# Kernel optimization log

Hardware: AMD Instinct MI355X
Metric: run time of the kernel (lower is better)

The kernel has to match this reference:

```python
import jax, jax.numpy as jnp
import numpy as np

B, T, D, H = 2, 2048, 1024, 16
HD = D // H  # head_dim = 64


def setup_inputs() -> dict:
    key = jax.random.key(0)
    ks = jax.random.split(key, 9)
    s = 0.02
    return {
        "hidden_states": jax.random.normal(ks[0], (B, T, D), jnp.float32),
        "attention_mask": jnp.zeros((B, 1, T, T), jnp.float32),
        "Wq": jax.random.normal(ks[1], (D, D), jnp.float32) * s,
        "bq": jax.random.normal(ks[2], (D,), jnp.float32) * s,
        "Wk": jax.random.normal(ks[3], (D, D), jnp.float32) * s,
        "bk": jax.random.normal(ks[4], (D,), jnp.float32) * s,
        "Wv": jax.random.normal(ks[5], (D, D), jnp.float32) * s,
        "bv": jax.random.normal(ks[6], (D,), jnp.float32) * s,
        "Wo": jax.random.normal(ks[7], (D, D), jnp.float32) * s,
        "bo": jax.random.normal(ks[8], (D,), jnp.float32) * s,
    }


def _heads(x):
    # [B, T, D] -> [B, H, T, HD]
    return x.reshape(B, -1, H, HD).transpose(0, 2, 1, 3)


def reference(hidden_states, attention_mask, Wq, bq, Wk, bk, Wv, bv, Wo, bo):
    scaling = HD ** -0.5
    # nn.Linear: x @ W.T + b; query scaled BEFORE head split (as in source)
    q = _heads((hidden_states @ Wq.T + bq) * scaling)  # [B,H,T,HD]
    k = _heads(hidden_states @ Wk.T + bk)
    v = _heads(hidden_states @ Wv.T + bv)
    # eager QK^T -> +mask -> softmax -> @V (full [B,H,T,T] materialized)
    attn = jnp.einsum('bhqd,bhkd->bhqk', q, k) + attention_mask
    attn = jax.nn.softmax(attn, axis=-1)
    out = jnp.einsum('bhqk,bhkd->bhqd', attn, v)  # [B,H,T,HD]
    out = out.transpose(0, 2, 1, 3).reshape(B, -1, D)
    return out @ Wo.T + bo
```

## Files before the change

kernel.cpp:

```cpp
#include <hip/hip_runtime.h>
#include <hip/hip_bf16.h>

typedef __bf16 v8bf __attribute__((ext_vector_type(8)));
typedef unsigned short v8us __attribute__((ext_vector_type(8)));
typedef float v4f __attribute__((ext_vector_type(4)));

#define B_ 2
#define T_ 2048
#define D_ 1024
#define H_ 16
#define HD_ 64
#define M_ 4096
#define LDST 88
#define PSTR 72

static __device__ __forceinline__ unsigned short f2bfbits(float f) {
    __hip_bfloat16 h = __float2bfloat16(f);
    unsigned short u;
    __builtin_memcpy(&u, &h, 2);
    return u;
}

static __device__ __forceinline__ v8us load8_f32_to_bf16(const float* g) {
    float4 fa = *(const float4*)g;
    float4 fb = *(const float4*)(g + 4);
    v8us p;
    p[0] = f2bfbits(fa.x); p[1] = f2bfbits(fa.y);
    p[2] = f2bfbits(fa.z); p[3] = f2bfbits(fa.w);
    p[4] = f2bfbits(fb.x); p[5] = f2bfbits(fb.y);
    p[6] = f2bfbits(fb.z); p[7] = f2bfbits(fb.w);
    return p;
}

static __device__ __forceinline__ void async16(const void* g, void* l) {
    __builtin_amdgcn_global_load_lds(
        (const __attribute__((address_space(1))) void*)g,
        (__attribute__((address_space(3))) void*)l, 16, 0, 0);
}

__global__ __launch_bounds__(256) void cvt_f32_bf16(
    const float* __restrict__ src, __hip_bfloat16* __restrict__ dst) {
    int i = (blockIdx.x * 256 + threadIdx.x) * 8;
    *(v8us*)&dst[i] = load8_f32_to_bf16(&src[i]);
}

__global__ __launch_bounds__(256) void gemm_qkv(
    const __hip_bfloat16* __restrict__ A, const __hip_bfloat16* __restrict__ W,
    const float* __restrict__ bq_, const float* __restrict__ bk_,
    const float* __restrict__ bv_, __hip_bfloat16* __restrict__ qo,
    __hip_bfloat16* __restrict__ ko, __hip_bfloat16* __restrict__ vo) {
    __shared__ __hip_bfloat16 sA[128 * 64];
    __shared__ __hip_bfloat16 sW[128 * 64];
    const int tid = threadIdx.x;
    const int wid = tid >> 6, lane = tid & 63;
    const int quad = lane >> 4, lq = lane & 15;
    const int wm = wid & 1, wn = wid >> 1;
    const int n0 = blockIdx.x * 128, m0 = blockIdx.y * 128;
    const int mid = n0 >> 10;
    const float* bias = (mid == 0) ? bq_ : (mid == 1) ? bk_ : bv_;

    v4f acc[4][4] = {};

    for (int k0 = 0; k0 < 1024; k0 += 64) {
        __syncthreads();
        for (int it = 0; it < 8; ++it) {
            int Lc = it * 256 + tid;
            int l1 = Lc & 1023;
            int row = l1 >> 3, pos = l1 & 7;
            if (it < 4)
                async16(&A[(size_t)(m0 + row) * 1024 + k0 + ((pos ^ (row & 7)) * 8)],
                        &sA[l1 * 8]);
            else
                async16(&W[(size_t)(n0 + row) * 1024 + k0 + ((pos ^ (row & 7)) * 8)],
                        &sW[l1 * 8]);
        }
        __syncthreads();
        for (int c = 0; c < 2; ++c) {
            v8bf af[4], wf[4];
            for (int mf = 0; mf < 4; ++mf) {
                int row = wm * 64 + mf * 16 + lq;
                af[mf] = *(const v8bf*)&sA[row * 64 + (((c * 4 + quad) ^ (lq & 7)) * 8)];
            }
            for (int nf = 0; nf < 4; ++nf) {
                int row = wn * 64 + nf * 16 + lq;
                wf[nf] = *(const v8bf*)&sW[row * 64 + (((c * 4 + quad) ^ (lq & 7)) * 8)];
            }
            for (int mf = 0; mf < 4; ++mf)
                for (int nf = 0; nf < 4; ++nf)
                    acc[mf][nf] = __builtin_amdgcn_mfma_f32_16x16x32_bf16(
                        af[mf], wf[nf], acc[mf][nf], 0, 0, 0);
        }
    }

    for (int nf = 0; nf < 4; ++nf) {
        int n = n0 + wn * 64 + nf * 16 + lq;
        int nl = n & 1023;
        int hh = nl >> 6, dd = nl & 63;
        float bvv = bias[nl];
        for (int mf = 0; mf < 4; ++mf) {
            int mbase = m0 + wm * 64 + mf * 16 + quad * 4;
            int bb = mbase >> 11;
            if (mid == 2) {
                int t0 = mbase & 2047;
                ushort4 pk;
                pk.x = f2bfbits(acc[mf][nf][0] + bvv);
                pk.y = f2bfbits(acc[mf][nf][1] + bvv);
                pk.z = f2bfbits(acc[mf][nf][2] + bvv);
                pk.w = f2bfbits(acc[mf][nf][3] + bvv);
                *(ushort4*)&vo[(((size_t)(bb * H_ + hh)) * HD_ + dd) * T_ + t0] = pk;
            } else {
                __hip_bfloat16* dst = (mid == 0) ? qo : ko;
                float sc = (mid == 0) ? 0.125f : 1.0f;
                for (int r = 0; r < 4; ++r) {
                    int m = mbase + r;
                    int t = m & 2047;
                    dst[(((size_t)(bb * H_ + hh)) * T_ + t) * HD_ + dd] =
                        __float2bfloat16((acc[mf][nf][r] + bvv) * sc);
                }
            }
        }
    }
}

__global__ __launch_bounds__(256) void gemm_out(
    const __hip_bfloat16* __restrict__ A, const __hip_bfloat16* __restrict__ W,
    const float* __restrict__ bias, float* __restrict__ out) {
    __shared__ __hip_bfloat16 sA[128 * 64];
    __shared__ __hip_bfloat16 sW[64 * 64];
    const int tid = threadIdx.x;
    const int wid = tid >> 6, lane = tid & 63;
    const int quad = lane >> 4, lq = lane & 15;
    const int wm = wid & 1, wn = wid >> 1;
    const int n0 = blockIdx.x * 64, m0 = blockIdx.y * 128;

    v4f acc[4][2] = {};

    for (int k0 = 0; k0 < 1024; k0 += 64) {
        __syncthreads();
        for (int it = 0; it < 4; ++it) {
            int Lc = wid * 256 + it * 64 + lane;
            int row = Lc >> 3, pos = Lc & 7;
            async16(&A[(size_t)(m0 + row) * 1024 + k0 + ((pos ^ (row & 7)) * 8)],
                    &sA[Lc * 8]);
        }
        for (int it = 0; it < 2; ++it) {
            int Lc = wid * 128 + it * 64 + lane;
            int row = Lc >> 3, pos = Lc & 7;
            async16(&W[(size_t)(n0 + row) * 1024 + k0 + ((pos ^ (row & 7)) * 8)],
                    &sW[Lc * 8]);
        }
        __syncthreads();
        for (int c = 0; c < 2; ++c) {
            v8bf af[4], wf[2];
            for (int mf = 0; mf < 4; ++mf) {
                int row = wm * 64 + mf * 16 + lq;
                af[mf] = *(const v8bf*)&sA[row * 64 + (((c * 4 + quad) ^ (lq & 7)) * 8)];
            }
            for (int nf = 0; nf < 2; ++nf) {
                int row = wn * 32 + nf * 16 + lq;
                wf[nf] = *(const v8bf*)&sW[row * 64 + (((c * 4 + quad) ^ (lq & 7)) * 8)];
            }
            for (int mf = 0; mf < 4; ++mf)
                for (int nf = 0; nf < 2; ++nf)
                    acc[mf][nf] = __builtin_amdgcn_mfma_f32_16x16x32_bf16(
                        af[mf], wf[nf], acc[mf][nf], 0, 0, 0);
        }
    }
    for (int nf = 0; nf < 2; ++nf) {
        int n = n0 + wn * 32 + nf * 16 + lq;
        float bv = bias[n];
        for (int mf = 0; mf < 4; ++mf) {
            int mbase = m0 + wm * 64 + mf * 16 + quad * 4;
            for (int r = 0; r < 4; ++r)
                out[(size_t)(mbase + r) * 1024 + n] = acc[mf][nf][r] + bv;
        }
    }
}

template <int EPI, bool ABF16, bool WBF16>
__global__ __launch_bounds__(256) void gemm128(
    const void* __restrict__ Av, const void* __restrict__ Wv_,
    const float* __restrict__ bias, void* __restrict__ outv) {
    __shared__ __hip_bfloat16 sA[128 * LDST];
    __shared__ __hip_bfloat16 sW[128 * LDST];
    const int tid = threadIdx.x;
    const int wid = tid >> 6, lane = tid & 63;
    const int quad = lane >> 4, lq = lane & 15;
    const int wm = wid & 1, wn = wid >> 1;
    const int n0 = blockIdx.x * 128, m0 = blockIdx.y * 128;
    v4f acc[4][4] = {};
    for (int k0 = 0; k0 < 1024; k0 += 64) {
        __syncthreads();
        for (int i = 0; i < 4; ++i) {
            int f = i * 256 + tid;
            int row = f >> 3, ch = f & 7;
            if constexpr (ABF16) {
                const __hip_bfloat16* A = (const __hip_bfloat16*)Av;
                *(int4*)&sA[row * LDST + ch * 8] =
                    *(const int4*)&A[(size_t)(m0 + row) * 1024 + k0 + ch * 8];
            } else {
                const float* A = (const float*)Av;
                *(v8us*)&sA[row * LDST + ch * 8] =
                    load8_f32_to_bf16(&A[(size_t)(m0 + row) * 1024 + k0 + ch * 8]);
            }
            if constexpr (WBF16) {
                const __hip_bfloat16* W = (const __hip_bfloat16*)Wv_;
                *(int4*)&sW[row * LDST + ch * 8] =
                    *(const int4*)&W[(size_t)(n0 + row) * 1024 + k0 + ch * 8];
            } else {
                const float* W = (const float*)Wv_;
                *(v8us*)&sW[row * LDST + ch * 8] =
                    load8_f32_to_bf16(&W[(size_t)(n0 + row) * 1024 + k0 + ch * 8]);
            }
        }
        __syncthreads();
        for (int c = 0; c < 2; ++c) {
            v8bf af[4], wf[4];
            for (int mf = 0; mf < 4; ++mf)
                af[mf] = *(const v8bf*)&sA[(wm * 64 + mf * 16 + lq) * LDST + c * 32 + quad * 8];
            for (int nf = 0; nf < 4; ++nf)
                wf[nf] = *(const v8bf*)&sW[(wn * 64 + nf * 16 + lq) * LDST + c * 32 + quad * 8];
            for (int mf = 0; mf < 4; ++mf)
                for (int nf = 0; nf < 4; ++nf)
                    acc[mf][nf] = __builtin_amdgcn_mfma_f32_16x16x32_bf16(
                        af[mf], wf[nf], acc[mf][nf], 0, 0, 0);
        }
    }
    for (int nf = 0; nf < 4; ++nf) {
        int n = n0 + wn * 64 + nf * 16 + lq;
        float bv = bias[n];
        for (int mf = 0; mf < 4; ++mf) {
            int mbase = m0 + wm * 64 + mf * 16 + quad * 4;
            if constexpr (EPI == 2) {
                __hip_bfloat16* out = (__hip_bfloat16*)outv;
                int bb = mbase >> 11, t0 = mbase & 2047;
                int hh = n >> 6, dd = n & 63;
                ushort4 pk;
                pk.x = f2bfbits(acc[mf][nf][0] + bv);
                pk.y = f2bfbits(acc[mf][nf][1] + bv);
                pk.z = f2bfbits(acc[mf][nf][2] + bv);
                pk.w = f2bfbits(acc[mf][nf][3] + bv);
                *(ushort4*)&out[(((size_t)(bb * H_ + hh)) * HD_ + dd) * T_ + t0] = pk;
            } else {
                for (int r = 0; r < 4; ++r) {
                    int m = mbase + r;
                    float v = acc[mf][nf][r] + bv;
                    if constexpr (EPI == 0) {
                        __hip_bfloat16* out = (__hip_bfloat16*)outv;
                        v *= 0.125f;
                        int bb = m >> 11, t = m & 2047, hh = n >> 6, dd = n & 63;
                        out[(((size_t)(bb * H_ + hh)) * T_ + t) * HD_ + dd] = __float2bfloat16(v);
                    } else if constexpr (EPI == 1) {
                        __hip_bfloat16* out = (__hip_bfloat16*)outv;
                        int bb = m >> 11, t = m & 2047, hh = n >> 6, dd = n & 63;
                        out[(((size_t)(bb * H_ + hh)) * T_ + t) * HD_ + dd] = __float2bfloat16(v);
                    } else {
                        float* out = (float*)outv;
                        out[(size_t)m * 1024 + n] = v;
                    }
                }
            }
        }
    }
}

__global__ __launch_bounds__(256) void attn_kernel(
    const __hip_bfloat16* __restrict__ q, const __hip_bfloat16* __restrict__ k,
    const __hip_bfloat16* __restrict__ vt, const float* __restrict__ mask,
    __hip_bfloat16* __restrict__ out) {
    __shared__ __hip_bfloat16 sK[64 * 64];
    __shared__ __hip_bfloat16 sV[64 * 64];
    __shared__ __hip_bfloat16 pT[4][32 * PSTR];
    const int tid = threadIdx.x;
    const int wid = tid >> 6, lane = tid & 63;
    const int quad = lane >> 4, lq = lane & 15;
    const int bh = blockIdx.y;
    const int b = bh >> 4, h = bh & 15;
    const int qb = blockIdx.x * 128 + wid * 32;
    const int qt0 = qb + lq, qt1 = qt0 + 16;

    v8bf bq0[2], bq1[2];
    for (int c = 0; c < 2; ++c) {
        bq0[c] = *(const v8bf*)&q[((size_t)bh * T_ + qt0) * HD_ + c * 32 + quad * 8];
        bq1[c] = *(const v8bf*)&q[((size_t)bh * T_ + qt1) * HD_ + c * 32 + quad * 8];
    }
    const float* mrow0 = mask + ((size_t)b * T_ + qt0) * T_;
    const float* mrow1 = mask + ((size_t)b * T_ + qt1) * T_;
    const __hip_bfloat16* kbase = k + (size_t)bh * T_ * HD_;
    const __hip_bfloat16* vbase = vt + (size_t)bh * HD_ * T_;

    float l0 = 0.f, l1 = 0.f;
    v4f o0[4] = {}, o1[4] = {};

    for (int kt0 = 0; kt0 < T_; kt0 += 64) {
        float4 mg0[4], mg1[4];
        for (int ki = 0; ki < 4; ++ki) {
            mg0[ki] = *(const float4*)&mrow0[kt0 + ki * 16 + quad * 4];
            mg1[ki] = *(const float4*)&mrow1[kt0 + ki * 16 + quad * 4];
        }
        __syncthreads();
        for (int it = 0; it < 2; ++it) {
            int Lc = wid * 128 + it * 64 + lane;
            int row = Lc >> 3, pos = Lc & 7;
            async16(&kbase[(size_t)(kt0 + row) * HD_ + ((pos ^ (row & 7)) * 8)],
                    &sK[Lc * 8]);
        }
        for (int it = 0; it < 2; ++it) {
            int Lc = wid * 128 + it * 64 + lane;
            int row = Lc >> 3, pos = Lc & 7;
            async16(&vbase[(size_t)row * T_ + kt0 + ((pos ^ (row & 7)) * 8)],
                    &sV[Lc * 8]);
        }
        __syncthreads();

        v4f st0[4] = {}, st1[4] = {};
        for (int ki = 0; ki < 4; ++ki)
            for (int c = 0; c < 2; ++c) {
                int row = ki * 16 + lq;
                v8bf ka = *(const v8bf*)&sK[row * 64 + (((c * 4 + quad) ^ (lq & 7)) * 8)];
                st0[ki] = __builtin_amdgcn_mfma_f32_16x16x32_bf16(ka, bq0[c], st0[ki], 0, 0, 0);
                st1[ki] = __builtin_amdgcn_mfma_f32_16x16x32_bf16(ka, bq1[c], st1[ki], 0, 0, 0);
            }
        for (int ki = 0; ki < 4; ++ki)
            for (int r = 0; r < 4; ++r) {
                st0[ki][r] = __expf(st0[ki][r] + (&mg0[ki].x)[r]);
                st1[ki][r] = __expf(st1[ki][r] + (&mg1[ki].x)[r]);
                l0 += st0[ki][r];
                l1 += st1[ki][r];
            }
        for (int ki = 0; ki < 4; ++ki) {
            ushort4 p0, p1;
            p0.x = f2bfbits(st0[ki][0]); p0.y = f2bfbits(st0[ki][1]);
            p0.z = f2bfbits(st0[ki][2]); p0.w = f2bfbits(st0[ki][3]);
            p1.x = f2bfbits(st1[ki][0]); p1.y = f2bfbits(st1[ki][1]);
            p1.z = f2bfbits(st1[ki][2]); p1.w = f2bfbits(st1[ki][3]);
            *(ushort4*)&pT[wid][lq * PSTR + ki * 16 + quad * 4] = p0;
            *(ushort4*)&pT[wid][(16 + lq) * PSTR + ki * 16 + quad * 4] = p1;
        }
        for (int c = 0; c < 2; ++c) {
            v8bf pb0 = *(const v8bf*)&pT[wid][lq * PSTR + c * 32 + quad * 8];
            v8bf pb1 = *(const v8bf*)&pT[wid][(16 + lq) * PSTR + c * 32 + quad * 8];
            for (int nt = 0; nt < 4; ++nt) {
                int row = nt * 16 + lq;
                v8bf va = *(const v8bf*)&sV[row * 64 + (((c * 4 + quad) ^ (lq & 7)) * 8)];
                o0[nt] = __builtin_amdgcn_mfma_f32_16x16x32_bf16(va, pb0, o0[nt], 0, 0, 0);
                o1[nt] = __builtin_amdgcn_mfma_f32_16x16x32_bf16(va, pb1, o1[nt], 0, 0, 0);
            }
        }
    }

    l0 += __shfl_xor(l0, 16); l0 += __shfl_xor(l0, 32);
    l1 += __shfl_xor(l1, 16); l1 += __shfl_xor(l1, 32);
    float i0 = 1.0f / l0, i1 = 1.0f / l1;
    for (int nt = 0; nt < 4; ++nt) {
        ushort4 p0, p1;
        p0.x = f2bfbits(o0[nt][0] * i0); p0.y = f2bfbits(o0[nt][1] * i0);
        p0.z = f2bfbits(o0[nt][2] * i0); p0.w = f2bfbits(o0[nt][3] * i0);
        p1.x = f2bfbits(o1[nt][0] * i1); p1.y = f2bfbits(o1[nt][1] * i1);
        p1.z = f2bfbits(o1[nt][2] * i1); p1.w = f2bfbits(o1[nt][3] * i1);
        *(ushort4*)&out[((size_t)b * T_ + qt0) * D_ + h * HD_ + nt * 16 + quad * 4] = p0;
        *(ushort4*)&out[((size_t)b * T_ + qt1) * D_ + h * HD_ + nt * 16 + quad * 4] = p1;
    }
}

extern "C" void kernel_launch(void* const* d_in, const int* in_sizes, int n_in,
                              void* d_out, int out_size, void* d_ws, size_t ws_size,
                              hipStream_t stream) {
    const float* hs   = (const float*)d_in[0];
    const float* mask = (const float*)d_in[1];
    const float* Wq   = (const float*)d_in[2];
    const float* bq   = (const float*)d_in[3];
    const float* Wk   = (const float*)d_in[4];
    const float* bk   = (const float*)d_in[5];
    const float* Wv   = (const float*)d_in[6];
    const float* bv   = (const float*)d_in[7];
    const float* Wo   = (const float*)d_in[8];
    const float* bo   = (const float*)d_in[9];
    float* out = (float*)d_out;

    const size_t TEN = (size_t)B_ * H_ * T_ * HD_;
    const size_t WEL = (size_t)D_ * D_;
    __hip_bfloat16* q_ws  = (__hip_bfloat16*)d_ws;
    __hip_bfloat16* k_ws  = q_ws + TEN;
    __hip_bfloat16* vt_ws = k_ws + TEN;
    __hip_bfloat16* at_ws = vt_ws + TEN;

    dim3 qkvgrid(3072 / 128, M_ / 128);
    dim3 outgrid(D_ / 64, M_ / 128);
    dim3 ogrid(D_ / 128, M_ / 128);
    dim3 agrid(T_ / 128, B_ * H_);

    const size_t need = (4 * TEN + TEN + 4 * WEL) * sizeof(__hip_bfloat16);
    if (ws_size >= need) {
        __hip_bfloat16* hsb = at_ws + TEN;
        __hip_bfloat16* wqb = hsb + TEN;
        __hip_bfloat16* wkb = wqb + WEL;
        __hip_bfloat16* wvb = wkb + WEL;
        __hip_bfloat16* wob = wvb + WEL;
        cvt_f32_bf16<<<(int)(TEN / 2048), 256, 0, stream>>>(hs, hsb);
        cvt_f32_bf16<<<(int)(WEL / 2048), 256, 0, stream>>>(Wq, wqb);
        cvt_f32_bf16<<<(int)(WEL / 2048), 256, 0, stream>>>(Wk, wkb);
        cvt_f32_bf16<<<(int)(WEL / 2048), 256, 0, stream>>>(Wv, wvb);
        cvt_f32_bf16<<<(int)(WEL / 2048), 256, 0, stream>>>(Wo, wob);
        gemm_qkv<<<qkvgrid, 256, 0, stream>>>(hsb, wqb, bq, bk, bv, q_ws, k_ws, vt_ws);
        attn_kernel<<<agrid, 256, 0, stream>>>(q_ws, k_ws, vt_ws, mask, at_ws);
        gemm_out<<<outgrid, 256, 0, stream>>>(at_ws, wob, bo, out);
    } else {
        gemm128<0, false, false><<<ogrid, 256, 0, stream>>>(hs, Wq, bq, q_ws);
        gemm128<1, false, false><<<ogrid, 256, 0, stream>>>(hs, Wk, bk, k_ws);
        gemm128<2, false, false><<<ogrid, 256, 0, stream>>>(hs, Wv, bv, vt_ws);
        attn_kernel<<<agrid, 256, 0, stream>>>(q_ws, k_ws, vt_ws, mask, at_ws);
        gemm128<3, true, false><<<ogrid, 256, 0, stream>>>(at_ws, Wo, bo, out);
    }
}
```

Baseline: 258.1 us.

## Enlarge attention KV tile to 128, fold log2e into Q, merge conversion launches

Each attention iteration now stages 128 keys and values in LDS instead of 64, which halves the number of barrier and load phases per query block. The inner loop is split into two 64-key halves, and the second half's mask is loaded after the first barrier to hide latency. The softmax scale now includes log2(e) in Q, so exp2f with an fma on the mask replaces __expf. The five f32-to-bf16 conversion launches are merged into one kernel. This costs twice the K/V LDS, which may lower occupancy, and the softmax still skips the running-max subtraction, so it could overflow on larger inputs.

Measured after the change: 262.5 us. No clear change (+1.7%).

```diff
diff --git a/kernel.cpp b/kernel.cpp
--- a/kernel.cpp
+++ b/kernel.cpp
@@ -13,6 +13,7 @@
 #define M_ 4096
 #define LDST 88
 #define PSTR 72
+#define LOG2E 1.44269504f
 
 static __device__ __forceinline__ unsigned short f2bfbits(float f) {
     __hip_bfloat16 h = __float2bfloat16(f);
@@ -38,9 +39,25 @@
         (__attribute__((address_space(3))) void*)l, 16, 0, 0);
 }
 
-__global__ __launch_bounds__(256) void cvt_f32_bf16(
-    const float* __restrict__ src, __hip_bfloat16* __restrict__ dst) {
-    int i = (blockIdx.x * 256 + threadIdx.x) * 8;
+__global__ __launch_bounds__(256) void cvt_multi(
+    const float* __restrict__ hs, const float* __restrict__ wq,
+    const float* __restrict__ wk, const float* __restrict__ wv,
+    const float* __restrict__ wo, __hip_bfloat16* __restrict__ hsb,
+    __hip_bfloat16* __restrict__ wqb, __hip_bfloat16* __restrict__ wkb,
+    __hip_bfloat16* __restrict__ wvb, __hip_bfloat16* __restrict__ wob) {
+    int bid = blockIdx.x;
+    const float* src;
+    __hip_bfloat16* dst;
+    int off;
+    if (bid < 2048) {
+        src = hs; dst = hsb; off = bid;
+    } else {
+        int w = (bid - 2048) >> 9;
+        off = (bid - 2048) & 511;
+        src = (w == 0) ? wq : (w == 1) ? wk : (w == 2) ? wv : wo;
+        dst = (w == 0) ? wqb : (w == 1) ? wkb : (w == 2) ? wvb : wob;
+    }
+    int i = (off * 256 + threadIdx.x) * 8;
     *(v8us*)&dst[i] = load8_f32_to_bf16(&src[i]);
 }
 
@@ -110,7 +127,7 @@
                 *(ushort4*)&vo[(((size_t)(bb * H_ + hh)) * HD_ + dd) * T_ + t0] = pk;
             } else {
                 __hip_bfloat16* dst = (mid == 0) ? qo : ko;
-                float sc = (mid == 0) ? 0.125f : 1.0f;
+                float sc = (mid == 0) ? 0.125f * LOG2E : 1.0f;
                 for (int r = 0; r < 4; ++r) {
                     int m = mbase + r;
                     int t = m & 2047;
@@ -247,7 +264,7 @@
                     float v = acc[mf][nf][r] + bv;
                     if constexpr (EPI == 0) {
                         __hip_bfloat16* out = (__hip_bfloat16*)outv;
-                        v *= 0.125f;
+                        v *= 0.125f * LOG2E;
                         int bb = m >> 11, t = m & 2047, hh = n >> 6, dd = n & 63;
                         out[(((size_t)(bb * H_ + hh)) * T_ + t) * HD_ + dd] = __float2bfloat16(v);
                     } else if constexpr (EPI == 1) {
@@ -268,8 +285,8 @@
     const __hip_bfloat16* __restrict__ q, const __hip_bfloat16* __restrict__ k,
     const __hip_bfloat16* __restrict__ vt, const float* __restrict__ mask,
     __hip_bfloat16* __restrict__ out) {
-    __shared__ __hip_bfloat16 sK[64 * 64];
-    __shared__ __hip_bfloat16 sV[64 * 64];
+    __shared__ __hip_bfloat16 sK[128 * 64];
+    __shared__ __hip_bfloat16 sV[64 * 128];
     __shared__ __hip_bfloat16 pT[4][32 * PSTR];
     const int tid = threadIdx.x;
     const int wid = tid >> 6, lane = tid & 63;
@@ -292,59 +309,71 @@
     float l0 = 0.f, l1 = 0.f;
     v4f o0[4] = {}, o1[4] = {};
 
-    for (int kt0 = 0; kt0 < T_; kt0 += 64) {
-        float4 mg0[4], mg1[4];
+    for (int kt0 = 0; kt0 < T_; kt0 += 128) {
+        float4 ma0[4], ma1[4];
         for (int ki = 0; ki < 4; ++ki) {
-            mg0[ki] = *(const float4*)&mrow0[kt0 + ki * 16 + quad * 4];
-            mg1[ki] = *(const float4*)&mrow1[kt0 + ki * 16 + quad * 4];
-        }
-        __syncthreads();
-        for (int it = 0; it < 2; ++it) {
-            int Lc = wid * 128 + it * 64 + lane;
+            ma0[ki] = *(const float4*)&mrow0[kt0 + ki * 16 + quad * 4];
+            ma1[ki] = *(const float4*)&mrow1[kt0 + ki * 16 + quad * 4];
+        }
+        __syncthreads();
+        for (int it = 0; it < 4; ++it) {
+            int Lc = it * 256 + tid;
             int row = Lc >> 3, pos = Lc & 7;
             async16(&kbase[(size_t)(kt0 + row) * HD_ + ((pos ^ (row & 7)) * 8)],
                     &sK[Lc * 8]);
         }
-        for (int it = 0; it < 2; ++it) {
-            int Lc = wid * 128 + it * 64 + lane;
-            int row = Lc >> 3, pos = Lc & 7;
-            async16(&vbase[(size_t)row * T_ + kt0 + ((pos ^ (row & 7)) * 8)],
+        for (int it = 0; it < 4; ++it) {
+            int Lc = it * 256 + tid;
+            int row = Lc >> 4, pos = Lc & 15;
+            async16(&vbase[(size_t)row * T_ + kt0 + ((pos ^ (row & 15)) * 8)],
                     &sV[Lc * 8]);
         }
         __syncthreads();
 
-        v4f st0[4] = {}, st1[4] = {};
-        for (int ki = 0; ki < 4; ++ki)
+        float4 mb0[4], mb1[4];
+        for (int ki = 0; ki < 4; ++ki) {
+            mb0[ki] = *(const float4*)&mrow0[kt0 + 64 + ki * 16 + quad * 4];
+            mb1[ki] = *(const float4*)&mrow1[kt0 + 64 + ki * 16 + quad * 4];
+        }
+
+        for (int hf = 0; hf < 2; ++hf) {
+            const int ko = hf * 64;
+            float4* mg0 = hf ? mb0 : ma0;
+            float4* mg1 = hf ? mb1 : ma1;
+            v4f st0[4] = {}, st1[4] = {};
+            for (int ki = 0; ki < 4; ++ki)
+                for (int c = 0; c < 2; ++c) {
+                    int row = ko + ki * 16 + lq;
+                    v8bf ka = *(const v8bf*)&sK[row * 64 + (((c * 4 + quad) ^ (row & 7)) * 8)];
+                    st0[ki] = __builtin_amdgcn_mfma_f32_16x16x32_bf16(ka, bq0[c], st0[ki], 0, 0, 0);
+                    st1[ki] = __builtin_amdgcn_mfma_f32_16x16x32_bf16(ka, bq1[c], st1[ki], 0, 0, 0);
+                }
+            for (int ki = 0; ki < 4; ++ki)
+                for (int r = 0; r < 4; ++r) {
+                    st0[ki][r] = exp2f(fmaf((&mg0[ki].x)[r], LOG2E, st0[ki][r]));
+                    st1[ki][r] = exp2f(fmaf((&mg1[ki].x)[r], LOG2E, st1[ki][r]));
+                    l0 += st0[ki][r];
+                    l1 += st1[ki][r];
+                }
+            for (int ki = 0; ki < 4; ++ki) {
+                ushort4 p0, p1;
+                p0.x = f2bfbits(st0[ki][0]); p0.y = f2bfbits(st0[ki][1]);
+                p0.z = f2bfbits(st0[ki][2]); p0.w = f2bfbits(st0[ki][3]);
+                p1.x = f2bfbits(st1[ki][0]); p1.y = f2bfbits(st1[ki][1]);
+                p1.z = f2bfbits(st1[ki][2]); p1.w = f2bfbits(st1[ki][3]);
+                *(ushort4*)&pT[wid][lq * PSTR + ki * 16 + quad * 4] = p0;
+                *(ushort4*)&pT[wid][(16 + lq) * PSTR + ki * 16 + quad * 4] = p1;
+            }
             for (int c = 0; c < 2; ++c) {
-                int row = ki * 16 + lq;
-                v8bf ka = *(const v8bf*)&sK[row * 64 + (((c * 4 + quad) ^ (lq & 7)) * 8)];
-                st0[ki] = __builtin_amdgcn_mfma_f32_16x16x32_bf16(ka, bq0[c], st0[ki], 0, 0, 0);
-                st1[ki] = __builtin_amdgcn_mfma_f32_16x16x32_bf16(ka, bq1[c], st1[ki], 0, 0, 0);
-            }
-        for (int ki = 0; ki < 4; ++ki)
-            for (int r = 0; r < 4; ++r) {
-                st0[ki][r] = __expf(st0[ki][r] + (&mg0[ki].x)[r]);
-                st1[ki][r] = __expf(st1[ki][r] + (&mg1[ki].x)[r]);
-                l0 += st0[ki][r];
-                l1 += st1[ki][r];
-            }
-        for (int ki = 0; ki < 4; ++ki) {
-            ushort4 p0, p1;
-            p0.x = f2bfbits(st0[ki][0]); p0.y = f2bfbits(st0[ki][1]);
-            p0.z = f2bfbits(st0[ki][2]); p0.w = f2bfbits(st0[ki][3]);
-            p1.x = f2bfbits(st1[ki][0]); p1.y = f2bfbits(st1[ki][1]);
-            p1.z = f2bfbits(st1[ki][2]); p1.w = f2bfbits(st1[ki][3]);
-            *(ushort4*)&pT[wid][lq * PSTR + ki * 16 + quad * 4] = p0;
-            *(ushort4*)&pT[wid][(16 + lq) * PSTR + ki * 16 + quad * 4] = p1;
-        }
-        for (int c = 0; c < 2; ++c) {
-            v8bf pb0 = *(const v8bf*)&pT[wid][lq * PSTR + c * 32 + quad * 8];
-            v8bf pb1 = *(const v8bf*)&pT[wid][(16 + lq) * PSTR + c * 32 + quad * 8];
-            for (int nt = 0; nt < 4; ++nt) {
-                int row = nt * 16 + lq;
-                v8bf va = *(const v8bf*)&sV[row * 64 + (((c * 4 + quad) ^ (lq & 7)) * 8)];
-                o0[nt] = __builtin_amdgcn_mfma_f32_16x16x32_bf16(va, pb0, o0[nt], 0, 0, 0);
-                o1[nt] = __builtin_amdgcn_mfma_f32_16x16x32_bf16(va, pb1, o1[nt], 0, 0, 0);
+                v8bf pb0 = *(const v8bf*)&pT[wid][lq * PSTR + c * 32 + quad * 8];
+                v8bf pb1 = *(const v8bf*)&pT[wid][(16 + lq) * PSTR + c * 32 + quad * 8];
+                for (int nt = 0; nt < 4; ++nt) {
+                    int row = nt * 16 + lq;
+                    int cs = hf * 8 + c * 4 + quad;
+                    v8bf va = *(const v8bf*)&sV[row * 128 + ((cs ^ (row & 15)) * 8)];
+                    o0[nt] = __builtin_amdgcn_mfma_f32_16x16x32_bf16(va, pb0, o0[nt], 0, 0, 0);
+                    o1[nt] = __builtin_amdgcn_mfma_f32_16x16x32_bf16(va, pb1, o1[nt], 0, 0, 0);
+                }
             }
         }
     }
@@ -397,11 +426,8 @@
         __hip_bfloat16* wkb = wqb + WEL;
         __hip_bfloat16* wvb = wkb + WEL;
         __hip_bfloat16* wob = wvb + WEL;
-        cvt_f32_bf16<<<(int)(TEN / 2048), 256, 0, stream>>>(hs, hsb);
-        cvt_f32_bf16<<<(int)(WEL / 2048), 256, 0, stream>>>(Wq, wqb);
-        cvt_f32_bf16<<<(int)(WEL / 2048), 256, 0, stream>>>(Wk, wkb);
-        cvt_f32_bf16<<<(int)(WEL / 2048), 256, 0, stream>>>(Wv, wvb);
-        cvt_f32_bf16<<<(int)(WEL / 2048), 256, 0, stream>>>(Wo, wob);
+        cvt_multi<<<2048 + 4 * 512, 256, 0, stream>>>(hs, Wq, Wk, Wv, Wo,
+                                                      hsb, wqb, wkb, wvb, wob);
         gemm_qkv<<<qkvgrid, 256, 0, stream>>>(hsb, wqb, bq, bk, bv, q_ws, k_ws, vt_ws);
         attn_kernel<<<agrid, 256, 0, stream>>>(q_ws, k_ws, vt_ws, mask, at_ws);
         gemm_out<<<outgrid, 256, 0, stream>>>(at_ws, wob, bo, out);
```
